# Kernel optimization log

Measured on AMD Instinct MI355X. Metric: run time of the kernel, lower is better.

## Reference

```python
import jax, jax.numpy as jnp
import numpy as np

DIM = 1024
NUM_HEADS = 16
HEAD_DIM = DIM // NUM_HEADS
SCALE = HEAD_DIM ** -0.5


def setup_inputs() -> dict:
    key = jax.random.key(0)
    ks = jax.random.split(key, 12)
    B, N, M, C = 4, 512, 2048, DIM
    x = jax.random.normal(ks[0], (B, N, C), dtype=jnp.float32)
    context = jax.random.normal(ks[1], (B, M, C), dtype=jnp.float32)
    mask = jax.random.randint(ks[2], (B, M), 0, 2, dtype=jnp.int32)
    mask = mask.at[:, 0].set(1)  # ensure at least one valid key per row
    w = 0.02
    Wq = jax.random.normal(ks[3], (C, C), dtype=jnp.float32) * w
    bq = jnp.zeros((C,), dtype=jnp.float32)
    Wk = jax.random.normal(ks[4], (C, C), dtype=jnp.float32) * w
    bk = jnp.zeros((C,), dtype=jnp.float32)
    Wv = jax.random.normal(ks[5], (C, C), dtype=jnp.float32) * w
    bv = jnp.zeros((C,), dtype=jnp.float32)
    Wo = jax.random.normal(ks[6], (C, C), dtype=jnp.float32) * w
    bo = jnp.zeros((C,), dtype=jnp.float32)
    return {"x": x, "context": context, "ctx_key_padding_mask": mask,
            "Wq": Wq, "bq": bq, "Wk": Wk, "bk": bk,
            "Wv": Wv, "bv": bv, "Wo": Wo, "bo": bo}


def reference(x, context, ctx_key_padding_mask, Wq, bq, Wk, bk, Wv, bv, Wo, bo):
    B, N, C = x.shape
    M = context.shape[1]
    H, D = NUM_HEADS, HEAD_DIM
    # torch nn.Linear: y = x @ W.T + b
    q = (x @ Wq.T + bq).reshape(B, N, H, D)
    k = (context @ Wk.T + bk).reshape(B, M, H, D)
    v = (context @ Wv.T + bv).reshape(B, M, H, D)
    scores = jnp.einsum('bnhd,bmhd->bhnm', q, k) * SCALE  # [B,H,N,M]
    neg = jnp.finfo(scores.dtype).min
    bias = jnp.where(ctx_key_padding_mask[:, None, None, :] != 0, 0.0, neg).astype(scores.dtype)
    attn = jax.nn.softmax(scores + bias, axis=-1)
    out = jnp.einsum('bhnm,bmhd->bnhd', attn, v).reshape(B, N, C)
    return out @ Wo.T + bo
```

## Files before the change

kernel.cpp:

```cpp
#include <hip/hip_runtime.h>
#include <hip/hip_bf16.h>
#include <stdint.h>


typedef __attribute__((ext_vector_type(4))) float f32x4;
typedef __attribute__((ext_vector_type(8))) __bf16 bf16x8;
typedef __attribute__((ext_vector_type(8))) unsigned short u16x8;

#define DEVI __device__ __forceinline__

#define QSC (0.125f * 1.44269504088896f)

DEVI f32x4 mfma16(u16x8 a, u16x8 b, f32x4 c) {
  return __builtin_amdgcn_mfma_f32_16x16x32_bf16(
      __builtin_bit_cast(bf16x8, a), __builtin_bit_cast(bf16x8, b), c, 0, 0, 0);
}

DEVI unsigned short f2bf(float f) {
  union { float f; unsigned int u; } x; x.f = f;
  unsigned int u = x.u;
  return (unsigned short)((u + 0x7fffu + ((u >> 16) & 1u)) >> 16);
}

DEVI float exp2_fast(float x) {
#if __has_builtin(__builtin_amdgcn_exp2f)
  return __builtin_amdgcn_exp2f(x);
#else
  return exp2f(x);
#endif
}

DEVI void llds16(const void* g, void* l) {
  __builtin_amdgcn_global_load_lds(
      (const __attribute__((address_space(1))) void*)g,
      (__attribute__((address_space(3))) void*)l, 16, 0, 0);
}

__global__ __launch_bounds__(256)
void cast_fused(const float* __restrict__ x, const float* __restrict__ ctx,
                const float* __restrict__ wq, const float* __restrict__ wk,
                const float* __restrict__ wv, const float* __restrict__ wo,
                unsigned short* __restrict__ xb, unsigned short* __restrict__ cb,
                unsigned short* __restrict__ wqb, unsigned short* __restrict__ wkb,
                unsigned short* __restrict__ wvb, unsigned short* __restrict__ wob) {
  int bid = blockIdx.x;
  const float* src; unsigned short* dst; float scale = 1.f;
  if (bid < 2048)        { src = x;   dst = xb; }
  else if (bid < 10240)  { src = ctx; dst = cb;  bid -= 2048; }
  else if (bid < 11264)  { src = wq;  dst = wqb; bid -= 10240; scale = QSC; }
  else if (bid < 12288)  { src = wk;  dst = wkb; bid -= 11264; }
  else if (bid < 13312)  { src = wv;  dst = wvb; bid -= 12288; }
  else                   { src = wo;  dst = wob; bid -= 13312; }
  int idx = (bid * 256 + threadIdx.x) * 4;
  const float4 v = *(const float4*)(src + idx);
  ushort4 o;
  o.x = f2bf(v.x * scale); o.y = f2bf(v.y * scale);
  o.z = f2bf(v.z * scale); o.w = f2bf(v.w * scale);
  *(ushort4*)(dst + idx) = o;
}

DEVI void epi_store(f32x4 (&acc)[4][4], const float* __restrict__ bias,
                    float bscale, void* __restrict__ Cout,
                    int bm, int bn, int logS, int mode,
                    unsigned short* cst, int tid, int wave, int l15, int quad) {
  const int wm = wave & 1, wn = wave >> 1;
  __syncthreads();
  for (int half = 0; half < 2; ++half) {
    if (wm == half) {
#pragma unroll
      for (int mi = 0; mi < 4; ++mi)
#pragma unroll
        for (int ni = 0; ni < 4; ++ni)
#pragma unroll
          for (int r = 0; r < 4; ++r) {
            int lrow = mi * 16 + quad * 4 + r;
            int lcol = wn * 64 + ni * 16 + l15;
            unsigned short bv = f2bf(acc[mi][ni][r] + bias[bn + lcol] * bscale);
            if (mode == 0) cst[lrow * 136 + lcol] = bv;
            else           cst[lcol * 72 + lrow] = bv;
          }
    }
    __syncthreads();
    if (mode == 0) {
      int lrow = tid >> 2, cc = (tid & 3) * 32;
      int row = bm + half * 64 + lrow;
      int b = row >> logS, sl = row & ((1 << logS) - 1);
#pragma unroll
      for (int j = 0; j < 4; ++j) {
        int col = bn + cc + j * 8;
        int h = col >> 6, d = col & 63;
        *(u16x8*)&((unsigned short*)Cout)[(((size_t)(b * 16 + h) << logS) + sl) * 64 + d] =
            *(const u16x8*)&cst[lrow * 136 + cc + j * 8];
      }
    } else {
      int c = tid >> 1, rc = (tid & 1) * 32;
      int gc = bn + c, h = gc >> 6, d = gc & 63;
      int b = bm >> 11;
      size_t base = ((size_t)(b * 16 + h) * 64 + d) * 2048 + (bm & 2047) + half * 64 + rc;
#pragma unroll
      for (int j = 0; j < 4; ++j)
        *(u16x8*)&((unsigned short*)Cout)[base + j * 8] =
            *(const u16x8*)&cst[c * 72 + rc + j * 8];
    }
    __syncthreads();
  }
}

DEVI void kv_body(const unsigned short* __restrict__ A,
                  const unsigned short* __restrict__ WK,
                  const unsigned short* __restrict__ WV,
                  const float* __restrict__ bk, const float* __restrict__ bv,
                  unsigned short* __restrict__ kh, unsigned short* __restrict__ vt,
                  int bm, int bn, unsigned short* sh) {
  constexpr int K = 1024;
  unsigned short* As = sh;
  unsigned short* Ks = sh + 128 * 64;
  unsigned short* Vs = sh + 2 * 128 * 64;

  const int tid = threadIdx.x;
  const int wave = tid >> 6, lane = tid & 63;
  const int l15 = lane & 15, quad = lane >> 4;
  const int wm = wave & 1, wn = wave >> 1;

  f32x4 ak[4][4] = {}, av[4][4] = {};

  for (int k0 = 0; k0 < K; k0 += 64) {
    __syncthreads();
#pragma unroll
    for (int c = 0; c < 4; ++c) {
      int s = c * 256 + tid;
      int m = s >> 3;
      int k8 = (s & 7) ^ (m & 7);
      llds16(A + (size_t)(bm + m) * K + k0 + k8 * 8, &As[s * 8]);
      llds16(WK + (size_t)(bn + m) * K + k0 + k8 * 8, &Ks[s * 8]);
      llds16(WV + (size_t)(bn + m) * K + k0 + k8 * 8, &Vs[s * 8]);
    }
    __syncthreads();
#pragma unroll
    for (int ks = 0; ks < 2; ++ks) {
      const int k8 = ks * 4 + quad;
      u16x8 af[4], bf[4];
#pragma unroll
      for (int i = 0; i < 4; ++i) {
        int m = wm * 64 + i * 16 + l15;
        af[i] = *(const u16x8*)(&As[(m * 8 + (k8 ^ (m & 7))) * 8]);
      }
#pragma unroll
      for (int i = 0; i < 4; ++i) {
        int n = wn * 64 + i * 16 + l15;
        bf[i] = *(const u16x8*)(&Ks[(n * 8 + (k8 ^ (n & 7))) * 8]);
      }
#pragma unroll
      for (int mi = 0; mi < 4; ++mi)
#pragma unroll
        for (int ni = 0; ni < 4; ++ni)
          ak[mi][ni] = mfma16(af[mi], bf[ni], ak[mi][ni]);
#pragma unroll
      for (int i = 0; i < 4; ++i) {
        int n = wn * 64 + i * 16 + l15;
        bf[i] = *(const u16x8*)(&Vs[(n * 8 + (k8 ^ (n & 7))) * 8]);
      }
#pragma unroll
      for (int mi = 0; mi < 4; ++mi)
#pragma unroll
        for (int ni = 0; ni < 4; ++ni)
          av[mi][ni] = mfma16(af[mi], bf[ni], av[mi][ni]);
    }
  }

  epi_store(ak, bk, 1.f, kh, bm, bn, 11, 0, sh, tid, wave, l15, quad);
  epi_store(av, bv, 1.f, vt, bm, bn, 11, 2, sh, tid, wave, l15, quad);
}

DEVI void q_body(const unsigned short* __restrict__ A,
                 const unsigned short* __restrict__ W,
                 const float* __restrict__ bias,
                 unsigned short* __restrict__ Cout,
                 int bm, int bn, unsigned short* sh) {
  constexpr int K = 1024;
  unsigned short* As = sh;
  unsigned short* Bs = sh + 128 * 64;

  const int tid = threadIdx.x;
  const int wave = tid >> 6, lane = tid & 63;
  const int l15 = lane & 15, quad = lane >> 4;
  const int wm = wave & 1, wn = wave >> 1;

  f32x4 acc[4][4] = {};

  for (int k0 = 0; k0 < K; k0 += 64) {
    __syncthreads();
#pragma unroll
    for (int c = 0; c < 4; ++c) {
      int s = c * 256 + tid;
      int m = s >> 3;
      int k8 = (s & 7) ^ (m & 7);
      llds16(A + (size_t)(bm + m) * K + k0 + k8 * 8, &As[s * 8]);
      llds16(W + (size_t)(bn + m) * K + k0 + k8 * 8, &Bs[s * 8]);
    }
    __syncthreads();
#pragma unroll
    for (int ks = 0; ks < 2; ++ks) {
      const int k8 = ks * 4 + quad;
      u16x8 af[4], bf[4];
#pragma unroll
      for (int i = 0; i < 4; ++i) {
        int m = wm * 64 + i * 16 + l15;
        af[i] = *(const u16x8*)(&As[(m * 8 + (k8 ^ (m & 7))) * 8]);
        int n = wn * 64 + i * 16 + l15;
        bf[i] = *(const u16x8*)(&Bs[(n * 8 + (k8 ^ (n & 7))) * 8]);
      }
#pragma unroll
      for (int mi = 0; mi < 4; ++mi)
#pragma unroll
        for (int ni = 0; ni < 4; ++ni)
          acc[mi][ni] = mfma16(af[mi], bf[ni], acc[mi][ni]);
    }
  }

  epi_store(acc, bias, QSC, Cout, bm, bn, 9, 0, sh, tid, wave, l15, quad);
}

__global__ __launch_bounds__(256, 2)
void gemm_qkv(const unsigned short* __restrict__ xb,
              const unsigned short* __restrict__ cb,
              const unsigned short* __restrict__ wq,
              const unsigned short* __restrict__ wk,
              const unsigned short* __restrict__ wv,
              const float* __restrict__ bq, const float* __restrict__ bk,
              const float* __restrict__ bv,
              unsigned short* __restrict__ qh, unsigned short* __restrict__ kh,
              unsigned short* __restrict__ vt) {
  __shared__ __align__(16) unsigned short sh[128 * 64 * 3];
  const int x = blockIdx.x, y = blockIdx.y;
  if (y < 8) {
    kv_body(cb, wk, wv, bk, bv, kh, vt, x * 128, y * 128, sh);
  } else {
    q_body(xb, wq, bq, qh, (x & 15) * 128, (y - 8) * 512 + (x >> 4) * 128, sh);
  }
}

__global__ __launch_bounds__(256)
void gemm_o(const unsigned short* __restrict__ A,
            const unsigned short* __restrict__ W,
            const float* __restrict__ bo, float* __restrict__ out) {
  constexpr int K = 1024;
  __shared__ __align__(16) unsigned short As[64 * 64];
  __shared__ __align__(16) unsigned short Bs[128 * 64];

  const int tid = threadIdx.x;
  const int wave = tid >> 6, lane = tid & 63;
  const int l15 = lane & 15, quad = lane >> 4;
  const int bm = blockIdx.x * 64, bn = blockIdx.y * 128;

  f32x4 acc[4][2] = {};

  for (int k0 = 0; k0 < K; k0 += 64) {
    __syncthreads();
#pragma unroll
    for (int c = 0; c < 2; ++c) {
      int s = c * 256 + tid;
      int m = s >> 3, k8 = (s & 7) ^ (m & 7);
      llds16(A + (size_t)(bm + m) * K + k0 + k8 * 8, &As[s * 8]);
    }
#pragma unroll
    for (int c = 0; c < 4; ++c) {
      int s = c * 256 + tid;
      int m = s >> 3, k8 = (s & 7) ^ (m & 7);
      llds16(W + (size_t)(bn + m) * K + k0 + k8 * 8, &Bs[s * 8]);
    }
    __syncthreads();
#pragma unroll
    for (int ks = 0; ks < 2; ++ks) {
      const int k8 = ks * 4 + quad;
      u16x8 af[4], bf[2];
#pragma unroll
      for (int i = 0; i < 4; ++i) {
        int m = i * 16 + l15;
        af[i] = *(const u16x8*)(&As[(m * 8 + (k8 ^ (m & 7))) * 8]);
      }
#pragma unroll
      for (int i = 0; i < 2; ++i) {
        int n = wave * 32 + i * 16 + l15;
        bf[i] = *(const u16x8*)(&Bs[(n * 8 + (k8 ^ (n & 7))) * 8]);
      }
#pragma unroll
      for (int mi = 0; mi < 4; ++mi)
#pragma unroll
        for (int ni = 0; ni < 2; ++ni)
          acc[mi][ni] = mfma16(af[mi], bf[ni], acc[mi][ni]);
    }
  }

#pragma unroll
  for (int mi = 0; mi < 4; ++mi)
#pragma unroll
    for (int ni = 0; ni < 2; ++ni)
#pragma unroll
      for (int r = 0; r < 4; ++r) {
        int row = bm + mi * 16 + quad * 4 + r;
        int col = bn + wave * 32 + ni * 16 + l15;
        out[(size_t)row * 1024 + col] = acc[mi][ni][r] + bo[col];
      }
}

#define PS 72
__global__ __launch_bounds__(256, 2)
void attn_kernel(const unsigned short* __restrict__ Q,
                 const unsigned short* __restrict__ K,
                 const unsigned short* __restrict__ Vt,
                 const int* __restrict__ mask,
                 unsigned short* __restrict__ O) {
  __shared__ float bias_lds[2048];
  __shared__ __align__(16) unsigned short p_lds[4][2][16 * PS];
  __shared__ float l_lds[4][64];
  __shared__ __align__(16) float o_comb[64][68];

  const int tid = threadIdx.x;
  const int wave = tid >> 6, lane = tid & 63;
  const int l15 = lane & 15, quad = lane >> 4;
  const int bh = blockIdx.x, b = bh >> 4, h = bh & 15;
  const int q0 = blockIdx.y * 64;

  {
    const int* mb = mask + b * 2048;
    for (int i = tid; i < 2048; i += 256)
      bias_lds[i] = mb[i] ? -8.f : -1e30f;
  }
  __syncthreads();

  const unsigned short* Qb = Q + ((size_t)bh * 512 + q0) * 64;
  const unsigned short* Kb = K + (size_t)bh * (2048 * 64);
  const unsigned short* Vb = Vt + (size_t)bh * (64 * 2048);

  u16x8 aq[4][2];
#pragma unroll
  for (int qg = 0; qg < 4; ++qg)
#pragma unroll
    for (int ks = 0; ks < 2; ++ks)
      aq[qg][ks] = *(const u16x8*)(Qb + (qg * 16 + l15) * 64 + ks * 32 + quad * 8);

  f32x4 o_acc[4][4] = {};
  float l_s[4] = {0.f, 0.f, 0.f, 0.f};

  u16x8 kf[2][4];

  auto load_k = [&](int kb) {
#pragma unroll
    for (int ns = 0; ns < 4; ++ns)
#pragma unroll
      for (int ks = 0; ks < 2; ++ks)
        kf[ks][ns] = *(const u16x8*)(Kb + (size_t)(kb + ns * 16 + l15) * 64 + ks * 32 + quad * 8);
  };

  load_k(wave * 64);

#pragma unroll 1
  for (int t = 0; t < 8; ++t) {
    const int kb = wave * 64 + t * 256;
    const int kb_next = kb + (t < 7 ? 256 : 0);

    u16x8 vf[2][4];
#pragma unroll
    for (int nd = 0; nd < 4; ++nd)
#pragma unroll
      for (int ks = 0; ks < 2; ++ks)
        vf[ks][nd] = *(const u16x8*)(Vb + (size_t)(nd * 16 + l15) * 2048 + kb + ks * 32 + quad * 8);
    f32x4 bfr[4];
#pragma unroll
    for (int ns = 0; ns < 4; ++ns)
      bfr[ns] = *(const f32x4*)&bias_lds[kb + ns * 16 + quad * 4];

#pragma unroll
    for (int qg = 0; qg < 4; ++qg) {
      f32x4 sfr[4];
#pragma unroll
      for (int ns = 0; ns < 4; ++ns) {
        f32x4 sa = bfr[ns];
#pragma unroll
        for (int ks = 0; ks < 2; ++ks)
          sa = mfma16(kf[ks][ns], aq[qg][ks], sa);
        sfr[ns] = sa;
      }

      if (qg == 3) load_k(kb_next);

      float rsum = 0.f;
#pragma unroll
      for (int ns = 0; ns < 4; ++ns) {
        unsigned int pr[4];
#pragma unroll
        for (int r = 0; r < 4; ++r) {
          float p = exp2_fast(sfr[ns][r]);
          unsigned int u = __builtin_bit_cast(unsigned int, p) & 0xffff0000u;
          rsum += __builtin_bit_cast(float, u);
          pr[r] = u;
        }
        uint2 pw;
        pw.x = __builtin_amdgcn_perm(pr[1], pr[0], 0x07060302u);
        pw.y = __builtin_amdgcn_perm(pr[3], pr[2], 0x07060302u);
        *(uint2*)&p_lds[wave][qg & 1][l15 * PS + ns * 16 + quad * 4] = pw;
      }
      rsum += __shfl_xor(rsum, 16, 64);
      rsum += __shfl_xor(rsum, 32, 64);
      l_s[qg] += rsum;

#pragma unroll
      for (int ks = 0; ks < 2; ++ks) {
        u16x8 pf = *(const u16x8*)&p_lds[wave][qg & 1][l15 * PS + ks * 32 + quad * 8];
#pragma unroll
        for (int nd = 0; nd < 4; ++nd)
          o_acc[qg][nd] = mfma16(pf, vf[ks][nd], o_acc[qg][nd]);
      }
    }
  }

  if (quad == 0) {
#pragma unroll
    for (int qg = 0; qg < 4; ++qg)
      l_lds[wave][qg * 16 + l15] = l_s[qg];
  }
  __syncthreads();

  for (int w = 0; w < 4; ++w) {
    if (wave == w) {
#pragma unroll
      for (int qg = 0; qg < 4; ++qg)
#pragma unroll
        for (int r = 0; r < 4; ++r) {
          const int q = qg * 16 + quad * 4 + r;
#pragma unroll
          for (int nd = 0; nd < 4; ++nd) {
            const int d = nd * 16 + l15;
            float v = o_acc[qg][nd][r];
            if (w == 0) o_comb[q][d] = v;
            else        o_comb[q][d] += v;
          }
        }
    }
    __syncthreads();
  }

  {
    const int q = tid >> 2, dc = (tid & 3) * 16;
    const float inv = 1.f / (l_lds[0][q] + l_lds[1][q] + l_lds[2][q] + l_lds[3][q]);
    unsigned short* Ob = O + ((size_t)(b * 512 + q0 + q)) * 1024 + h * 64 + dc;
    u16x8 o1, o2;
#pragma unroll
    for (int j = 0; j < 8; ++j) o1[j] = f2bf(o_comb[q][dc + j] * inv);
#pragma unroll
    for (int j = 0; j < 8; ++j) o2[j] = f2bf(o_comb[q][dc + 8 + j] * inv);
    *(u16x8*)(Ob) = o1;
    *(u16x8*)(Ob + 8) = o2;
  }
}

extern "C" void kernel_launch(void* const* d_in, const int* in_sizes, int n_in,
                              void* d_out, int out_size, void* d_ws, size_t ws_size,
                              hipStream_t stream) {
  const float* x   = (const float*)d_in[0];
  const float* ctx = (const float*)d_in[1];
  const int* mask  = (const int*)d_in[2];
  const float* Wq  = (const float*)d_in[3];
  const float* bq  = (const float*)d_in[4];
  const float* Wk  = (const float*)d_in[5];
  const float* bk  = (const float*)d_in[6];
  const float* Wv  = (const float*)d_in[7];
  const float* bv  = (const float*)d_in[8];
  const float* Wo  = (const float*)d_in[9];
  const float* bo  = (const float*)d_in[10];

  char* ws = (char*)d_ws;
  unsigned short* xb  = (unsigned short*)(ws + ((size_t)0  << 20));
  unsigned short* cb  = (unsigned short*)(ws + ((size_t)4  << 20));
  unsigned short* wqb = (unsigned short*)(ws + ((size_t)20 << 20));
  unsigned short* wkb = (unsigned short*)(ws + ((size_t)22 << 20));
  unsigned short* wvb = (unsigned short*)(ws + ((size_t)24 << 20));
  unsigned short* wob = (unsigned short*)(ws + ((size_t)26 << 20));
  unsigned short* qh  = (unsigned short*)(ws + ((size_t)28 << 20));
  unsigned short* kh  = (unsigned short*)(ws + ((size_t)32 << 20));
  unsigned short* vt  = (unsigned short*)(ws + ((size_t)48 << 20));
  unsigned short* ah  = (unsigned short*)(ws + ((size_t)64 << 20));

  cast_fused<<<14336, 256, 0, stream>>>(x, ctx, Wq, Wk, Wv, Wo,
                                        xb, cb, wqb, wkb, wvb, wob);
  gemm_qkv<<<dim3(64, 10), 256, 0, stream>>>(xb, cb, wqb, wkb, wvb,
                                             bq, bk, bv, qh, kh, vt);
  attn_kernel<<<dim3(64, 8), 256, 0, stream>>>(qh, kh, vt, mask, ah);
  gemm_o<<<dim3(32, 8), 256, 0, stream>>>(ah, wob, bo, (float*)d_out);
}
```

Before: 215.2 us.

## Store Q/K/Vt in MFMA-fragment-tiled layout for coalesced attention loads

The projection epilogue now writes Q, K and transposed V in a tiled layout where each 16-row group's 8-element chunks are laid out contiguously per lane. The attention kernel reads its MFMA fragments from matching offsets, so the 64 lanes of a wave touch one contiguous 1 KB block instead of strided rows. This targets uncoalesced global loads in the attention inner loop. The attention kernel's launch bounds also drop to one block per SIMD, which frees more registers at the possible cost of occupancy. Scattered epilogue stores may cost a little more in the projection kernel.

```diff
diff --git a/kernel.cpp b/kernel.cpp
--- a/kernel.cpp
+++ b/kernel.cpp
@@ -84,23 +84,30 @@
     if (mode == 0) {
       int lrow = tid >> 2, cc = (tid & 3) * 32;
       int row = bm + half * 64 + lrow;
-      int b = row >> logS, sl = row & ((1 << logS) - 1);
+      int S = 1 << logS;
+      int b = row >> logS, sl = row & (S - 1);
 #pragma unroll
       for (int j = 0; j < 4; ++j) {
         int col = bn + cc + j * 8;
-        int h = col >> 6, d = col & 63;
-        *(u16x8*)&((unsigned short*)Cout)[(((size_t)(b * 16 + h) << logS) + sl) * 64 + d] =
+        int h = col >> 6, d8 = (col & 63) >> 3;
+        size_t base = (((size_t)(b * 16 + h)) << logS) * 64 +
+                      (size_t)(sl >> 4) * 1024 + d8 * 128 + (sl & 15) * 8;
+        *(u16x8*)&((unsigned short*)Cout)[base] =
             *(const u16x8*)&cst[lrow * 136 + cc + j * 8];
       }
     } else {
       int c = tid >> 1, rc = (tid & 1) * 32;
       int gc = bn + c, h = gc >> 6, d = gc & 63;
       int b = bm >> 11;
-      size_t base = ((size_t)(b * 16 + h) * 64 + d) * 2048 + (bm & 2047) + half * 64 + rc;
-#pragma unroll
-      for (int j = 0; j < 4; ++j)
-        *(u16x8*)&((unsigned short*)Cout)[base + j * 8] =
+#pragma unroll
+      for (int j = 0; j < 4; ++j) {
+        int key = (bm & 2047) + half * 64 + rc + j * 8;
+        size_t base = (size_t)(b * 16 + h) * 131072 +
+                      (size_t)(((key >> 6) * 4 + (d >> 4)) * 8 + ((key >> 3) & 7)) * 128 +
+                      (d & 15) * 8;
+        *(u16x8*)&((unsigned short*)Cout)[base] =
             *(const u16x8*)&cst[c * 72 + rc + j * 8];
+      }
     }
     __syncthreads();
   }
@@ -305,7 +312,7 @@
 }
 
 #define PS 72
-__global__ __launch_bounds__(256, 2)
+__global__ __launch_bounds__(256, 1)
 void attn_kernel(const unsigned short* __restrict__ Q,
                  const unsigned short* __restrict__ K,
                  const unsigned short* __restrict__ Vt,
@@ -329,16 +336,16 @@
   }
   __syncthreads();
 
-  const unsigned short* Qb = Q + ((size_t)bh * 512 + q0) * 64;
-  const unsigned short* Kb = K + (size_t)bh * (2048 * 64);
-  const unsigned short* Vb = Vt + (size_t)bh * (64 * 2048);
+  const unsigned short* Qb = Q + (size_t)bh * 32768 + (size_t)(q0 >> 4) * 1024;
+  const unsigned short* Kb = K + (size_t)bh * 131072;
+  const unsigned short* Vb = Vt + (size_t)bh * 131072;
 
   u16x8 aq[4][2];
 #pragma unroll
   for (int qg = 0; qg < 4; ++qg)
 #pragma unroll
     for (int ks = 0; ks < 2; ++ks)
-      aq[qg][ks] = *(const u16x8*)(Qb + (qg * 16 + l15) * 64 + ks * 32 + quad * 8);
+      aq[qg][ks] = *(const u16x8*)(Qb + ((qg * 8 + ks * 4 + quad) * 16 + l15) * 8);
 
   f32x4 o_acc[4][4] = {};
   float l_s[4] = {0.f, 0.f, 0.f, 0.f};
@@ -346,11 +353,12 @@
   u16x8 kf[2][4];
 
   auto load_k = [&](int kb) {
+    const int kg0 = kb >> 4;
 #pragma unroll
     for (int ns = 0; ns < 4; ++ns)
 #pragma unroll
       for (int ks = 0; ks < 2; ++ks)
-        kf[ks][ns] = *(const u16x8*)(Kb + (size_t)(kb + ns * 16 + l15) * 64 + ks * 32 + quad * 8);
+        kf[ks][ns] = *(const u16x8*)(Kb + (((size_t)(kg0 + ns) * 8 + ks * 4 + quad) * 16 + l15) * 8);
   };
 
   load_k(wave * 64);
@@ -361,11 +369,12 @@
     const int kb_next = kb + (t < 7 ? 256 : 0);
 
     u16x8 vf[2][4];
+    const int kt4 = (kb >> 6) * 4;
 #pragma unroll
     for (int nd = 0; nd < 4; ++nd)
 #pragma unroll
       for (int ks = 0; ks < 2; ++ks)
-        vf[ks][nd] = *(const u16x8*)(Vb + (size_t)(nd * 16 + l15) * 2048 + kb + ks * 32 + quad * 8);
+        vf[ks][nd] = *(const u16x8*)(Vb + (((size_t)(kt4 + nd) * 8 + ks * 4 + quad) * 16 + l15) * 8);
     f32x4 bfr[4];
 #pragma unroll
     for (int ns = 0; ns < 4; ++ns)
```

After: 212.0 us. About the same (-1.5%).
